# Optimization experiments

Hardware: AMD Instinct MI355X
Metric: run time of the kernel (lower is better)

The kernel has to match this reference:

```python
import jax, jax.numpy as jnp
import numpy as np

N = 131072          # number of feature vectors
F_DIM = 512         # feature_dim
D = 256             # latent_dim
K = 2048            # num_embeddings
BETA = 0.25         # commitment_cost


def _mlp(x, params):
    # params: list of (W, b); ReLU after every layer (matches nn.Sequential)
    for W, b in params:
        x = jax.nn.relu(x @ W + b)
    return x


def setup_inputs() -> dict:
    key = jax.random.key(0)
    ks = jax.random.split(key, 14)

    def lin(k, fan_in, fan_out):
        bound = 1.0 / np.sqrt(fan_in)
        kw, kb = jax.random.split(k)
        W = jax.random.uniform(kw, (fan_in, fan_out), jnp.float32, -bound, bound)
        b = jax.random.uniform(kb, (fan_out,), jnp.float32, -bound, bound)
        return W, b

    enc_w1, enc_b1 = lin(ks[1], F_DIM, 64)
    enc_w2, enc_b2 = lin(ks[2], 64, 128)
    enc_w3, enc_b3 = lin(ks[3], 128, D)
    dec_w1, dec_b1 = lin(ks[4], D, 128)
    dec_w2, dec_b2 = lin(ks[5], 128, 64)
    dec_w3, dec_b3 = lin(ks[6], 64, F_DIM)
    emb = jax.random.uniform(ks[7], (K, D), jnp.float32, -1.0 / K, 1.0 / K)
    x = jax.random.normal(ks[0], (N, F_DIM), jnp.float32)
    return {
        "x": x,
        "enc_w1": enc_w1, "enc_b1": enc_b1,
        "enc_w2": enc_w2, "enc_b2": enc_b2,
        "enc_w3": enc_w3, "enc_b3": enc_b3,
        "dec_w1": dec_w1, "dec_b1": dec_b1,
        "dec_w2": dec_w2, "dec_b2": dec_b2,
        "dec_w3": dec_w3, "dec_b3": dec_b3,
        "emb": emb,
    }


def reference(x, enc_w1, enc_b1, enc_w2, enc_b2, enc_w3, enc_b3,
              dec_w1, dec_b1, dec_w2, dec_b2, dec_w3, dec_b3, emb):
    enc = [(enc_w1, enc_b1), (enc_w2, enc_b2), (enc_w3, enc_b3)]
    dec = [(dec_w1, dec_b1), (dec_w2, dec_b2), (dec_w3, dec_b3)]

    z_e = _mlp(x, enc)  # (N, D)

    # ||z - e||^2 = ||z||^2 - 2 z.e + ||e||^2   (avoids (N,K,D) broadcast)
    z_sq = jnp.sum(z_e * z_e, axis=-1, keepdims=True)      # (N, 1)
    e_sq = jnp.sum(emb * emb, axis=-1)                      # (K,)
    distances = z_sq - 2.0 * (z_e @ emb.T) + e_sq           # (N, K)
    idx = jnp.argmin(distances, axis=1)                     # (N,)
    z_q = emb[idx]                                          # (N, D)

    commitment_loss = BETA * jnp.mean((jax.lax.stop_gradient(z_q) - z_e) ** 2)
    embedding_loss = jnp.mean((z_q - jax.lax.stop_gradient(z_e)) ** 2)
    quantization_loss = embedding_loss + commitment_loss

    # straight-through estimator
    z_q_st = z_e + jax.lax.stop_gradient(z_q - z_e)

    x_recon = _mlp(z_q_st, dec)
    recon_loss = jnp.mean((x_recon - x) ** 2)
    loss = recon_loss + quantization_loss

    z_latent = jax.lax.stop_gradient(z_q_st)
    return (z_latent, loss)
```

## Files before the change

### kernel.cpp

```cpp
#include <hip/hip_runtime.h>

#define NROWS 131072
#define KE 2048
#define CAND_CAP 8192

typedef unsigned long long u64_t;
typedef unsigned int u32;
typedef __attribute__((ext_vector_type(8))) short bf16x8;
typedef __attribute__((ext_vector_type(4))) float f32x4;

__device__ __forceinline__ unsigned f32_key(float f) {
  unsigned u = __float_as_uint(f);
  return (u & 0x80000000u) ? ~u : (u | 0x80000000u);
}

template <int MODE>
__global__ __launch_bounds__(256) void gemm64(
    const float* __restrict__ A, const float* __restrict__ B,
    const float* __restrict__ bias, float* __restrict__ C,
    int M, int N, int K,
    const int* __restrict__ gidx) {
  __shared__ __align__(16) float As[16][68];
  __shared__ __align__(16) float Bs[16][68];

  const int tid = threadIdx.x;
  const int tx = tid & 15;
  const int ty = tid >> 4;
  const int arow = blockIdx.x * 64;
  const int bcol = blockIdx.y * 64;

  const int lr = tid >> 2;
  const int lc = (tid & 3) * 4;
  int ga = arow + lr;
  if (MODE == 1) ga = gidx[ga];
  const float* Ap = A + (size_t)ga * K + lc;

  const int bkr = tid >> 4;
  const int bc4 = (tid & 15) * 4;
  const float* Bp = B + (size_t)bkr * N + bcol + bc4;

  float acc[4][4] = {};

  for (int kt = 0; kt < K; kt += 16) {
    float4 av = *reinterpret_cast<const float4*>(Ap);
    As[lc + 0][lr] = av.x;
    As[lc + 1][lr] = av.y;
    As[lc + 2][lr] = av.z;
    As[lc + 3][lr] = av.w;
    float4 bv = *reinterpret_cast<const float4*>(Bp);
    *reinterpret_cast<float4*>(&Bs[bkr][bc4]) = bv;
    Bp += (size_t)16 * N;
    Ap += 16;
    __syncthreads();
#pragma unroll
    for (int k = 0; k < 16; ++k) {
      float4 a = *reinterpret_cast<const float4*>(&As[k][ty * 4]);
      float4 b = *reinterpret_cast<const float4*>(&Bs[k][tx * 4]);
      acc[0][0] += a.x * b.x; acc[0][1] += a.x * b.y; acc[0][2] += a.x * b.z; acc[0][3] += a.x * b.w;
      acc[1][0] += a.y * b.x; acc[1][1] += a.y * b.y; acc[1][2] += a.y * b.z; acc[1][3] += a.y * b.w;
      acc[2][0] += a.z * b.x; acc[2][1] += a.z * b.y; acc[2][2] += a.z * b.z; acc[2][3] += a.z * b.w;
      acc[3][0] += a.w * b.x; acc[3][1] += a.w * b.y; acc[3][2] += a.w * b.z; acc[3][3] += a.w * b.w;
    }
    __syncthreads();
  }

#pragma unroll
  for (int i = 0; i < 4; ++i) {
    const int row = arow + ty * 4 + i;
    float4 v;
    v.x = fmaxf(acc[i][0] + bias[bcol + tx * 4 + 0], 0.f);
    v.y = fmaxf(acc[i][1] + bias[bcol + tx * 4 + 1], 0.f);
    v.z = fmaxf(acc[i][2] + bias[bcol + tx * 4 + 2], 0.f);
    v.w = fmaxf(acc[i][3] + bias[bcol + tx * 4 + 3], 0.f);
    *reinterpret_cast<float4*>(&C[(size_t)row * N + bcol + tx * 4]) = v;
  }
}

template <int MODE>
__global__ __launch_bounds__(256) void gemm128(
    const float* __restrict__ A, const float* __restrict__ B,
    const float* __restrict__ bias, float* __restrict__ C,
    int N, int K,
    const int* __restrict__ gidx,
    const float* __restrict__ X,
    float* __restrict__ parts) {
  __shared__ __align__(16) char smem[17408];
  float (*As)[132] = (float(*)[132])smem;
  float (*Bs)[132] = (float(*)[132])(smem + 8448);

  const int tid = threadIdx.x;
  const int tx = tid & 15;
  const int ty = tid >> 4;
  const int arow = blockIdx.x * 128;
  const int bcol = blockIdx.y * 128;

  const int r0 = tid >> 2;
  const int r1 = r0 + 64;
  const int lc = (tid & 3) * 4;
  int ga0 = arow + r0, ga1 = arow + r1;
  if (MODE == 1) { ga0 = gidx[ga0]; ga1 = gidx[ga1]; }
  const float* Ap0 = A + (size_t)ga0 * K + lc;
  const float* Ap1 = A + (size_t)ga1 * K + lc;

  const int bk0 = tid >> 5;
  const int bc0 = (tid & 31) * 4;
  const float* Bp0 = B + (size_t)bk0 * N + bcol + bc0;
  const float* Bp1 = B + (size_t)(bk0 + 8) * N + bcol + bc0;

  float acc[8][8] = {};

  for (int kt = 0; kt < K; kt += 16) {
    float4 a0 = *reinterpret_cast<const float4*>(Ap0);
    float4 a1 = *reinterpret_cast<const float4*>(Ap1);
    As[lc + 0][r0] = a0.x; As[lc + 1][r0] = a0.y; As[lc + 2][r0] = a0.z; As[lc + 3][r0] = a0.w;
    As[lc + 0][r1] = a1.x; As[lc + 1][r1] = a1.y; As[lc + 2][r1] = a1.z; As[lc + 3][r1] = a1.w;
    float4 b0 = *reinterpret_cast<const float4*>(Bp0);
    float4 b1 = *reinterpret_cast<const float4*>(Bp1);
    *reinterpret_cast<float4*>(&Bs[bk0][bc0]) = b0;
    *reinterpret_cast<float4*>(&Bs[bk0 + 8][bc0]) = b1;
    Bp0 += (size_t)16 * N; Bp1 += (size_t)16 * N;
    Ap0 += 16; Ap1 += 16;
    __syncthreads();
#pragma unroll
    for (int k = 0; k < 16; ++k) {
      float4 av0 = *reinterpret_cast<const float4*>(&As[k][ty * 4]);
      float4 av1 = *reinterpret_cast<const float4*>(&As[k][64 + ty * 4]);
      float4 bv0 = *reinterpret_cast<const float4*>(&Bs[k][tx * 4]);
      float4 bv1 = *reinterpret_cast<const float4*>(&Bs[k][64 + tx * 4]);
      const float a[8] = {av0.x, av0.y, av0.z, av0.w, av1.x, av1.y, av1.z, av1.w};
      const float b[8] = {bv0.x, bv0.y, bv0.z, bv0.w, bv1.x, bv1.y, bv1.z, bv1.w};
#pragma unroll
      for (int i = 0; i < 8; ++i)
#pragma unroll
        for (int j = 0; j < 8; ++j) acc[i][j] += a[i] * b[j];
    }
    __syncthreads();
  }

  if (MODE == 0 || MODE == 1) {
#pragma unroll
    for (int i = 0; i < 8; ++i) {
      const int row = arow + (i >> 2) * 64 + ty * 4 + (i & 3);
      const int c0 = bcol + tx * 4;
      const int c1 = bcol + 64 + tx * 4;
      float4 v0, v1;
      v0.x = fmaxf(acc[i][0] + bias[c0 + 0], 0.f);
      v0.y = fmaxf(acc[i][1] + bias[c0 + 1], 0.f);
      v0.z = fmaxf(acc[i][2] + bias[c0 + 2], 0.f);
      v0.w = fmaxf(acc[i][3] + bias[c0 + 3], 0.f);
      v1.x = fmaxf(acc[i][4] + bias[c1 + 0], 0.f);
      v1.y = fmaxf(acc[i][5] + bias[c1 + 1], 0.f);
      v1.z = fmaxf(acc[i][6] + bias[c1 + 2], 0.f);
      v1.w = fmaxf(acc[i][7] + bias[c1 + 3], 0.f);
      *reinterpret_cast<float4*>(&C[(size_t)row * N + c0]) = v0;
      *reinterpret_cast<float4*>(&C[(size_t)row * N + c1]) = v1;
    }
  } else if (MODE == 2) {
    float local = 0.f;
#pragma unroll
    for (int i = 0; i < 8; ++i) {
      const int row = arow + (i >> 2) * 64 + ty * 4 + (i & 3);
#pragma unroll
      for (int j = 0; j < 8; ++j) {
        const int col = bcol + (j >> 2) * 64 + tx * 4 + (j & 3);
        float v = fmaxf(acc[i][j] + bias[col], 0.f);
        float d = v - X[(size_t)row * N + col];
        local += d * d;
      }
    }
    float* rbuf = (float*)smem;
    rbuf[tid] = local;
    __syncthreads();
    for (int off = 128; off > 0; off >>= 1) {
      if (tid < off) rbuf[tid] += rbuf[tid + off];
      __syncthreads();
    }
    if (tid == 0) parts[blockIdx.y * gridDim.x + blockIdx.x] = rbuf[0];
  }
}

__device__ __forceinline__ unsigned short bf16_rne(float f) {
  unsigned u = __float_as_uint(f);
  u += 0x7FFFu + ((u >> 16) & 1u);
  return (unsigned short)(u >> 16);
}

__global__ __launch_bounds__(256) void cvt_z16t(const float* __restrict__ z_e,
                                                unsigned short* __restrict__ z16t) {
  const int c = blockIdx.x * 256 + threadIdx.x;
  const int lane = c & 63;
  const int kb = (c >> 6) & 7;
  const int fr = (c >> 9) & 3;
  const int w = (c >> 11) & 3;
  const int rowblk = c >> 13;
  const int row = rowblk * 256 + w * 64 + fr * 16 + (lane & 15);
  const int k0 = kb * 32 + (lane >> 4) * 8;
  const float* p = z_e + (size_t)row * 256 + k0;
  const float4 v0 = *reinterpret_cast<const float4*>(p);
  const float4 v1 = *reinterpret_cast<const float4*>(p + 4);
  const float f[8] = {v0.x, v0.y, v0.z, v0.w, v1.x, v1.y, v1.z, v1.w};
  unsigned short s[8];
#pragma unroll
  for (int j = 0; j < 8; ++j) s[j] = bf16_rne(f[j]);
  uint4 o;
  o.x = (u32)s[0] | ((u32)s[1] << 16);
  o.y = (u32)s[2] | ((u32)s[3] << 16);
  o.z = (u32)s[4] | ((u32)s[5] << 16);
  o.w = (u32)s[6] | ((u32)s[7] << 16);
  *reinterpret_cast<uint4*>(z16t + (size_t)c * 8) = o;
}

__global__ __launch_bounds__(256) void cvt_e16f(const float* __restrict__ emb,
                                                unsigned short* __restrict__ e16f) {
  const int c = blockIdx.x * 256 + threadIdx.x;
  const int l = c & 63;
  const int fc = (c >> 6) & 7;
  const int t = c >> 9;
  const int kb = t & 7;
  const int ct = t >> 3;
  const int col = ct * 128 + fc * 16 + (l & 15);
  const int k0 = kb * 32 + (l >> 4) * 8;
  const float* p = emb + (size_t)col * 256 + k0;
  const float4 v0 = *reinterpret_cast<const float4*>(p);
  const float4 v1 = *reinterpret_cast<const float4*>(p + 4);
  const float f[8] = {v0.x, v0.y, v0.z, v0.w, v1.x, v1.y, v1.z, v1.w};
  unsigned short s8[8];
#pragma unroll
  for (int j = 0; j < 8; ++j) s8[j] = bf16_rne(f[j]);
  uint4 o;
  o.x = (u32)s8[0] | ((u32)s8[1] << 16);
  o.y = (u32)s8[2] | ((u32)s8[3] << 16);
  o.z = (u32)s8[4] | ((u32)s8[5] << 16);
  o.w = (u32)s8[6] | ((u32)s8[7] << 16);
  *reinterpret_cast<uint4*>(e16f + (size_t)c * 8) = o;
}

__global__ __launch_bounds__(256, 1) void dist_g256(
    const unsigned short* __restrict__ z16t, const unsigned short* __restrict__ e16f,
    const float* __restrict__ zf, const float* __restrict__ ef,
    const float* __restrict__ zsq, const float* __restrict__ esq,
    const float* __restrict__ maxesq, u64_t* __restrict__ keys) {
  __shared__ float esq_lds[2048];
  __shared__ float me1_lds[256];
  __shared__ float rowmin_lds[256];
  __shared__ unsigned cand[CAND_CAP];
  __shared__ unsigned cnt;

  const int tid = threadIdx.x;
  const int l = tid & 63;
  const int w = tid >> 6;
  const int l15 = tid & 15;
  const int lk = (tid >> 4) & 3;
  const int arow = blockIdx.x * 256;

  if (tid == 0) cnt = 0;
  {
    for (int i = tid; i < 2048; i += 256) esq_lds[i] = esq[i];
    me1_lds[tid] = 0.009765625f * sqrtf(zsq[arow + tid]);
    rowmin_lds[tid] = 3.402823466e38f;
  }
  const float semax = sqrtf(maxesq[0]);

  bf16x8 a[4][8];
  {
    const char* zb = (const char*)z16t + (size_t)blockIdx.x * 131072 + w * 32768 + l * 16;
#pragma unroll
    for (int fr = 0; fr < 4; ++fr)
#pragma unroll
      for (int kb = 0; kb < 8; ++kb)
        a[fr][kb] = *reinterpret_cast<const bf16x8*>(zb + fr * 8192 + kb * 1024);
  }

  auto rescore = [&](unsigned e) {
    const int row = arow + (int)(e >> 11);
    const int col = (int)(e & 2047u);
    const float* zp = zf + (size_t)row * 256;
    const float* ep = ef + (size_t)col * 256;
    float p = 0.f;
#pragma unroll 8
    for (int k4 = 0; k4 < 256; k4 += 4) {
      const float4 zv = *reinterpret_cast<const float4*>(zp + k4);
      const float4 ev = *reinterpret_cast<const float4*>(ep + k4);
      p = fmaf(zv.x, ev.x, p);
      p = fmaf(zv.y, ev.y, p);
      p = fmaf(zv.z, ev.z, p);
      p = fmaf(zv.w, ev.w, p);
    }
    const float dsc = (zsq[row] - 2.f * p) + esq[col];
    const u64_t kk = ((u64_t)f32_key(dsc) << 32) | (unsigned)col;
    atomicMin(&keys[row], kk);
  };

  __syncthreads();

  const char* eb = (const char*)e16f + (size_t)l * 16;
  const int ct0 = (int)((blockIdx.x * 5u) & 15u);

  f32x4 acc[4][8];
#pragma unroll
  for (int fr = 0; fr < 4; ++fr)
#pragma unroll
    for (int fc = 0; fc < 8; ++fc) acc[fr][fc] = (f32x4){0.f, 0.f, 0.f, 0.f};

  bf16x8 bc[8], bn[8];
#pragma unroll
  for (int fc = 0; fc < 8; ++fc)
    bc[fc] = *reinterpret_cast<const bf16x8*>(eb + (size_t)(ct0 * 8) * 8192 + fc * 1024);

#pragma unroll 1
  for (int ctl = 0; ctl < 16; ++ctl) {
    const int ct = (ct0 + ctl) & 15;
#pragma unroll
    for (int kb = 0; kb < 8; ++kb) {
      const int nctl = (kb == 7) ? ctl + 1 : ctl;
      const int nkb = (kb == 7) ? 0 : kb + 1;
      if (nctl < 16) {
        const int nct = (ct0 + nctl) & 15;
        const char* tb = eb + (size_t)(nct * 8 + nkb) * 8192;
#pragma unroll
        for (int fc = 0; fc < 8; ++fc)
          bn[fc] = *reinterpret_cast<const bf16x8*>(tb + fc * 1024);
      }
#pragma unroll
      for (int fr = 0; fr < 4; ++fr)
#pragma unroll
        for (int fc = 0; fc < 8; ++fc)
          acc[fr][fc] = __builtin_amdgcn_mfma_f32_16x16x32_bf16(a[fr][kb], bc[fc], acc[fr][fc], 0, 0, 0);
#pragma unroll
      for (int fc = 0; fc < 8; ++fc) bc[fc] = bn[fc];
    }
    {
      float esqv[8], se[8];
#pragma unroll
      for (int fc = 0; fc < 8; ++fc) {
        esqv[fc] = esq_lds[ct * 128 + fc * 16 + l15];
        se[fc] = sqrtf(esqv[fc]);
      }
#pragma unroll
      for (int fr = 0; fr < 4; ++fr)
#pragma unroll
        for (int rg = 0; rg < 4; ++rg) {
          float s8[8];
          float lm = 3.402823466e38f;
#pragma unroll
          for (int fc = 0; fc < 8; ++fc) {
            s8[fc] = fmaf(-2.f, acc[fr][fc][rg], esqv[fc]);
            lm = fminf(lm, s8[fc]);
          }
#pragma unroll
          for (int m = 1; m < 16; m <<= 1) lm = fminf(lm, __shfl_xor(lm, m, 64));
          const int row = w * 64 + fr * 16 + lk * 4 + rg;
          const float rm = fminf(rowmin_lds[row], lm);
          if (l15 == 0) rowmin_lds[row] = rm;
          const float me1 = me1_lds[row];
#pragma unroll
          for (int fc = 0; fc < 8; ++fc) {
            const float thr = rm + me1 * (se[fc] + semax) + 1e-7f;
            if (s8[fc] <= thr) {
              const unsigned code =
                  ((unsigned)row << 11) | (unsigned)(ct * 128 + fc * 16 + l15);
              const unsigned idx = atomicAdd(&cnt, 1u);
              if (idx < CAND_CAP) cand[idx] = code;
              else rescore(code);
            }
          }
        }
#pragma unroll
      for (int fr = 0; fr < 4; ++fr)
#pragma unroll
        for (int fc = 0; fc < 8; ++fc) acc[fr][fc] = (f32x4){0.f, 0.f, 0.f, 0.f};
    }
  }

  __syncthreads();
  const unsigned nc = cnt < CAND_CAP ? cnt : CAND_CAP;
  for (unsigned i = tid; i < nc; i += 256) rescore(cand[i]);
}

__global__ __launch_bounds__(256) void max_esq(const float* __restrict__ esq,
                                               float* __restrict__ outv) {
  __shared__ float red[256];
  float m = 0.f;
  for (int i = threadIdx.x; i < KE; i += 256) m = fmaxf(m, esq[i]);
  red[threadIdx.x] = m;
  __syncthreads();
  for (int off = 128; off > 0; off >>= 1) {
    if (threadIdx.x < off) red[threadIdx.x] = fmaxf(red[threadIdx.x], red[threadIdx.x + off]);
    __syncthreads();
  }
  if (threadIdx.x == 0) outv[0] = red[0];
}

__global__ __launch_bounds__(256) void rowsq(const float* __restrict__ src,
                                             float* __restrict__ dst, int rows) {
  const int sub = threadIdx.x >> 6;
  const int lane = threadIdx.x & 63;
  const int r = blockIdx.x * 4 + sub;
  if (r >= rows) return;
  const float* p = src + (size_t)r * 256;
  float s = 0.f;
#pragma unroll
  for (int j = 0; j < 4; ++j) {
    float v = p[lane + 64 * j];
    s += v * v;
  }
#pragma unroll
  for (int off = 32; off > 0; off >>= 1) s += __shfl_down(s, off, 64);
  if (lane == 0) dst[r] = s;
}

__global__ __launch_bounds__(256) void init_keys(u64_t* __restrict__ keys) {
  keys[(size_t)blockIdx.x * 256 + threadIdx.x] = ~0ull;
}

__global__ __launch_bounds__(256) void gather_quant(
    const u64_t* __restrict__ keys, const float* __restrict__ emb,
    const float* __restrict__ z_e, float* __restrict__ zlat,
    int* __restrict__ idx_out, float* __restrict__ qparts) {
  const int sub = threadIdx.x >> 6;
  const int lane = threadIdx.x & 63;
  const int r = blockIdx.x * 4 + sub;
  const int idx = (int)(keys[r] & 0xFFFFFFFFull);
  if (lane == 0) idx_out[r] = idx;
  float s = 0.f;
#pragma unroll
  for (int j = 0; j < 4; ++j) {
    const int d = lane + 64 * j;
    float e = emb[(size_t)idx * 256 + d];
    float z = z_e[(size_t)r * 256 + d];
    float df = e - z;
    s += df * df;
    zlat[(size_t)r * 256 + d] = z + df;
  }
#pragma unroll
  for (int off = 32; off > 0; off >>= 1) s += __shfl_down(s, off, 64);
  __shared__ float red[4];
  if (lane == 0) red[sub] = s;
  __syncthreads();
  if (threadIdx.x == 0) qparts[blockIdx.x] = (red[0] + red[1]) + (red[2] + red[3]);
}

__global__ __launch_bounds__(256) void final_loss(
    const float* __restrict__ qparts, int nq,
    const float* __restrict__ rparts, int nr, float* __restrict__ out) {
  const int tid = threadIdx.x;
  double sq = 0.0, sr = 0.0;
  for (int i = tid; i < nq; i += 256) sq += (double)qparts[i];
  for (int i = tid; i < nr; i += 256) sr += (double)rparts[i];
  __shared__ double bq[256], br[256];
  bq[tid] = sq;
  br[tid] = sr;
  __syncthreads();
  for (int off = 128; off > 0; off >>= 1) {
    if (tid < off) {
      bq[tid] += bq[tid + off];
      br[tid] += br[tid + off];
    }
    __syncthreads();
  }
  if (tid == 0) {
    double qm = bq[0] / ((double)NROWS * 256.0);
    double rm = br[0] / ((double)NROWS * 512.0);
    out[(size_t)NROWS * 256] = (float)(rm + 1.25 * qm);
  }
}

extern "C" void kernel_launch(void* const* d_in, const int* in_sizes, int n_in,
                              void* d_out, int out_size, void* d_ws, size_t ws_size,
                              hipStream_t stream) {
  const float* x   = (const float*)d_in[0];
  const float* ew1 = (const float*)d_in[1];
  const float* eb1 = (const float*)d_in[2];
  const float* ew2 = (const float*)d_in[3];
  const float* eb2 = (const float*)d_in[4];
  const float* ew3 = (const float*)d_in[5];
  const float* eb3 = (const float*)d_in[6];
  const float* dw1 = (const float*)d_in[7];
  const float* db1 = (const float*)d_in[8];
  const float* dw2 = (const float*)d_in[9];
  const float* db2 = (const float*)d_in[10];
  const float* dw3 = (const float*)d_in[11];
  const float* db3 = (const float*)d_in[12];
  const float* emb = (const float*)d_in[13];

  char* ws = (char*)d_ws;
  float* h1            = (float*)(ws);
  unsigned short* e16f = (unsigned short*)(ws);
  float* maxesq        = (float*)(ws + 2097152ull);
  float* h2            = (float*)(ws + 33554432ull);
  unsigned short* z16t = (unsigned short*)(ws + 33554432ull);
  float* z_e    = (float*)(ws + 100663296ull);
  float* zsq    = (float*)(ws + 234881024ull);
  float* esq    = (float*)(ws + 235405312ull);
  u64_t* keys   = (u64_t*)(ws + 235413504ull);
  int* idx      = (int*)(ws + 236462080ull);
  float* qparts = (float*)(ws + 236986368ull);
  float* rparts = (float*)(ws + 237117440ull);

  float* out = (float*)d_out;
  dim3 blk(256);

  gemm64<0><<<dim3(NROWS / 64, 1), blk, 0, stream>>>(x, ew1, eb1, h1, NROWS, 64, 512,
      nullptr);
  gemm128<0><<<dim3(NROWS / 128, 1), blk, 0, stream>>>(h1, ew2, eb2, h2,
      128, 64, nullptr, nullptr, nullptr);
  gemm128<0><<<dim3(NROWS / 128, 2), blk, 0, stream>>>(h2, ew3, eb3, z_e,
      256, 128, nullptr, nullptr, nullptr);

  rowsq<<<dim3(NROWS / 4), blk, 0, stream>>>(z_e, zsq, NROWS);
  rowsq<<<dim3(KE / 4), blk, 0, stream>>>(emb, esq, KE);
  max_esq<<<dim3(1), blk, 0, stream>>>(esq, maxesq);
  init_keys<<<dim3(NROWS / 256), blk, 0, stream>>>(keys);

  cvt_z16t<<<dim3(NROWS * 256 / 8 / 256), blk, 0, stream>>>(z_e, z16t);
  cvt_e16f<<<dim3(KE * 256 / 8 / 256), blk, 0, stream>>>(emb, e16f);

  dist_g256<<<dim3(NROWS / 256), blk, 0, stream>>>(z16t, e16f, z_e, emb, zsq, esq,
      maxesq, keys);

  gather_quant<<<dim3(NROWS / 4), blk, 0, stream>>>(keys, emb, z_e, out, idx, qparts);

  gemm128<1><<<dim3(NROWS / 128, 1), blk, 0, stream>>>(emb, dw1, db1, h2,
      128, 256, idx, nullptr, nullptr);
  gemm64<0><<<dim3(NROWS / 64, 1), blk, 0, stream>>>(h2, dw2, db2, h1, NROWS, 64, 128,
      nullptr);
  gemm128<2><<<dim3(NROWS / 128, 4), blk, 0, stream>>>(h1, dw3, db3, nullptr,
      512, 64, nullptr, x, rparts);

  final_loss<<<dim3(1), blk, 0, stream>>>(qparts, NROWS / 4, rparts, 4096, out);
}
```

Baseline: 1.349 ms.

## Run decoder MLP layers on bf16 MFMA with pre-swizzled weight fragments

Replaces the three fp32 SIMT decoder GEMMs with a templated bf16 MFMA kernel. Weights are pre-converted into per-lane fragment layout and held in registers. The A tile is loaded into XOR-swizzled LDS, with the codebook gather fused in for the first layer. Intermediate activations are stored as bf16, which halves traffic, and the last layer fuses the reconstruction loss. This trades decoder precision (bf16 inputs and intermediates) for fewer FLOP-bound cycles and less memory traffic, so the loss may deviate slightly from the fp32 reference.

```diff
diff --git a/kernel.cpp b/kernel.cpp
--- a/kernel.cpp
+++ b/kernel.cpp
@@ -12,6 +12,12 @@
 __device__ __forceinline__ unsigned f32_key(float f) {
   unsigned u = __float_as_uint(f);
   return (u & 0x80000000u) ? ~u : (u | 0x80000000u);
+}
+
+__device__ __forceinline__ unsigned short bf16_rne(float f) {
+  unsigned u = __float_as_uint(f);
+  u += 0x7FFFu + ((u >> 16) & 1u);
+  return (unsigned short)(u >> 16);
 }
 
 template <int MODE>
@@ -137,52 +143,23 @@
     __syncthreads();
   }
 
-  if (MODE == 0 || MODE == 1) {
-#pragma unroll
-    for (int i = 0; i < 8; ++i) {
-      const int row = arow + (i >> 2) * 64 + ty * 4 + (i & 3);
-      const int c0 = bcol + tx * 4;
-      const int c1 = bcol + 64 + tx * 4;
-      float4 v0, v1;
-      v0.x = fmaxf(acc[i][0] + bias[c0 + 0], 0.f);
-      v0.y = fmaxf(acc[i][1] + bias[c0 + 1], 0.f);
-      v0.z = fmaxf(acc[i][2] + bias[c0 + 2], 0.f);
-      v0.w = fmaxf(acc[i][3] + bias[c0 + 3], 0.f);
-      v1.x = fmaxf(acc[i][4] + bias[c1 + 0], 0.f);
-      v1.y = fmaxf(acc[i][5] + bias[c1 + 1], 0.f);
-      v1.z = fmaxf(acc[i][6] + bias[c1 + 2], 0.f);
-      v1.w = fmaxf(acc[i][7] + bias[c1 + 3], 0.f);
-      *reinterpret_cast<float4*>(&C[(size_t)row * N + c0]) = v0;
-      *reinterpret_cast<float4*>(&C[(size_t)row * N + c1]) = v1;
-    }
-  } else if (MODE == 2) {
-    float local = 0.f;
-#pragma unroll
-    for (int i = 0; i < 8; ++i) {
-      const int row = arow + (i >> 2) * 64 + ty * 4 + (i & 3);
-#pragma unroll
-      for (int j = 0; j < 8; ++j) {
-        const int col = bcol + (j >> 2) * 64 + tx * 4 + (j & 3);
-        float v = fmaxf(acc[i][j] + bias[col], 0.f);
-        float d = v - X[(size_t)row * N + col];
-        local += d * d;
-      }
-    }
-    float* rbuf = (float*)smem;
-    rbuf[tid] = local;
-    __syncthreads();
-    for (int off = 128; off > 0; off >>= 1) {
-      if (tid < off) rbuf[tid] += rbuf[tid + off];
-      __syncthreads();
-    }
-    if (tid == 0) parts[blockIdx.y * gridDim.x + blockIdx.x] = rbuf[0];
-  }
-}
-
-__device__ __forceinline__ unsigned short bf16_rne(float f) {
-  unsigned u = __float_as_uint(f);
-  u += 0x7FFFu + ((u >> 16) & 1u);
-  return (unsigned short)(u >> 16);
+#pragma unroll
+  for (int i = 0; i < 8; ++i) {
+    const int row = arow + (i >> 2) * 64 + ty * 4 + (i & 3);
+    const int c0 = bcol + tx * 4;
+    const int c1 = bcol + 64 + tx * 4;
+    float4 v0, v1;
+    v0.x = fmaxf(acc[i][0] + bias[c0 + 0], 0.f);
+    v0.y = fmaxf(acc[i][1] + bias[c0 + 1], 0.f);
+    v0.z = fmaxf(acc[i][2] + bias[c0 + 2], 0.f);
+    v0.w = fmaxf(acc[i][3] + bias[c0 + 3], 0.f);
+    v1.x = fmaxf(acc[i][4] + bias[c1 + 0], 0.f);
+    v1.y = fmaxf(acc[i][5] + bias[c1 + 1], 0.f);
+    v1.z = fmaxf(acc[i][6] + bias[c1 + 2], 0.f);
+    v1.w = fmaxf(acc[i][7] + bias[c1 + 3], 0.f);
+    *reinterpret_cast<float4*>(&C[(size_t)row * N + c0]) = v0;
+    *reinterpret_cast<float4*>(&C[(size_t)row * N + c1]) = v1;
+  }
 }
 
 __global__ __launch_bounds__(256) void cvt_z16t(const float* __restrict__ z_e,
@@ -235,6 +212,46 @@
   *reinterpret_cast<uint4*>(e16f + (size_t)c * 8) = o;
 }
 
+__global__ __launch_bounds__(256) void cvt_rows16(const float* __restrict__ src,
+                                                  unsigned short* __restrict__ dst) {
+  const int i = blockIdx.x * 256 + threadIdx.x;
+  const float4 v0 = *reinterpret_cast<const float4*>(src + (size_t)i * 8);
+  const float4 v1 = *reinterpret_cast<const float4*>(src + (size_t)i * 8 + 4);
+  const float f[8] = {v0.x, v0.y, v0.z, v0.w, v1.x, v1.y, v1.z, v1.w};
+  unsigned short s[8];
+#pragma unroll
+  for (int j = 0; j < 8; ++j) s[j] = bf16_rne(f[j]);
+  uint4 o;
+  o.x = (u32)s[0] | ((u32)s[1] << 16);
+  o.y = (u32)s[2] | ((u32)s[3] << 16);
+  o.z = (u32)s[4] | ((u32)s[5] << 16);
+  o.w = (u32)s[6] | ((u32)s[7] << 16);
+  *reinterpret_cast<uint4*>(dst + (size_t)i * 8) = o;
+}
+
+__global__ __launch_bounds__(256) void cvt_w16f(const float* __restrict__ W,
+                                                unsigned short* __restrict__ Wf,
+                                                int N, int total) {
+  const int c = blockIdx.x * 256 + threadIdx.x;
+  if (c >= total) return;
+  const int l = c & 63;
+  const int f = c >> 6;
+  const int ng = N >> 4;
+  const int cg = f % ng;
+  const int kb = f / ng;
+  const int col = cg * 16 + (l & 15);
+  const int k0 = kb * 32 + ((l >> 4) & 3) * 8;
+  unsigned short s[8];
+#pragma unroll
+  for (int j = 0; j < 8; ++j) s[j] = bf16_rne(W[(size_t)(k0 + j) * N + col]);
+  uint4 o;
+  o.x = (u32)s[0] | ((u32)s[1] << 16);
+  o.y = (u32)s[2] | ((u32)s[3] << 16);
+  o.z = (u32)s[4] | ((u32)s[5] << 16);
+  o.w = (u32)s[6] | ((u32)s[7] << 16);
+  *reinterpret_cast<uint4*>(Wf + (size_t)c * 8) = o;
+}
+
 __global__ __launch_bounds__(256, 1) void dist_g256(
     const unsigned short* __restrict__ z16t, const unsigned short* __restrict__ e16f,
     const float* __restrict__ zf, const float* __restrict__ ef,
@@ -375,6 +392,112 @@
   __syncthreads();
   const unsigned nc = cnt < CAND_CAP ? cnt : CAND_CAP;
   for (unsigned i = tid; i < nc; i += 256) rescore(cand[i]);
+}
+
+template <int K, int NT, int NTOT, bool GATHER, bool LOSS>
+__global__ __launch_bounds__(256, 1) void dec_mfma(
+    const unsigned short* __restrict__ A16, const unsigned short* __restrict__ Wf,
+    const float* __restrict__ bias, unsigned short* __restrict__ C16,
+    const float* __restrict__ X, float* __restrict__ parts,
+    const int* __restrict__ gidx) {
+  constexpr int CH = K / 8;
+  constexpr int KB = K / 32;
+  constexpr int CG = NT / 16;
+  constexpr int NB = NTOT / NT;
+  __shared__ __align__(16) unsigned short Atile[128 * K];
+  __shared__ int idx_l[128];
+  __shared__ float rbuf[256];
+
+  const int tid = threadIdx.x;
+  const int l = tid & 63;
+  const int w = tid >> 6;
+  const int arow = (int)(blockIdx.x / NB) * 128;
+  const int bcol = (int)(blockIdx.x % NB) * NT;
+
+  if (GATHER) {
+    if (tid < 128) idx_l[tid] = gidx[arow + tid];
+    __syncthreads();
+  }
+  for (int q = tid; q < 128 * CH; q += 256) {
+    const int r = q / CH;
+    const int c = q % CH;
+    const unsigned short* src = GATHER
+        ? A16 + (size_t)idx_l[r] * K + c * 8
+        : A16 + (size_t)(arow + r) * K + c * 8;
+    const uint4 v = *reinterpret_cast<const uint4*>(src);
+    *reinterpret_cast<uint4*>(&Atile[(r * CH + (c ^ (r & 7))) * 8]) = v;
+  }
+
+  bf16x8 wf[KB][CG];
+#pragma unroll
+  for (int kb = 0; kb < KB; ++kb)
+#pragma unroll
+    for (int cg = 0; cg < CG; ++cg)
+      wf[kb][cg] = *reinterpret_cast<const bf16x8*>(
+          Wf + ((size_t)(kb * (NTOT / 16) + bcol / 16 + cg) * 64 + l) * 8);
+
+  __syncthreads();
+
+  f32x4 acc[2][CG];
+#pragma unroll
+  for (int fr = 0; fr < 2; ++fr)
+#pragma unroll
+    for (int cg = 0; cg < CG; ++cg) acc[fr][cg] = (f32x4){0.f, 0.f, 0.f, 0.f};
+
+#pragma unroll
+  for (int kb = 0; kb < KB; ++kb) {
+    bf16x8 af[2];
+#pragma unroll
+    for (int fr = 0; fr < 2; ++fr) {
+      const int r = w * 32 + fr * 16 + (l & 15);
+      const int c = (kb * 4 + ((l >> 4) & 3)) ^ (r & 7);
+      af[fr] = *reinterpret_cast<const bf16x8*>(&Atile[(r * CH + c) * 8]);
+    }
+#pragma unroll
+    for (int fr = 0; fr < 2; ++fr)
+#pragma unroll
+      for (int cg = 0; cg < CG; ++cg)
+        acc[fr][cg] = __builtin_amdgcn_mfma_f32_16x16x32_bf16(af[fr], wf[kb][cg], acc[fr][cg], 0, 0, 0);
+  }
+
+  if (!LOSS) {
+#pragma unroll
+    for (int fr = 0; fr < 2; ++fr)
+#pragma unroll
+      for (int cg = 0; cg < CG; ++cg) {
+        const int col = bcol + cg * 16 + (l & 15);
+        const float bv = bias[col];
+#pragma unroll
+        for (int rg = 0; rg < 4; ++rg) {
+          const int row = arow + w * 32 + fr * 16 + ((l >> 4) & 3) * 4 + rg;
+          const float v = fmaxf(acc[fr][cg][rg] + bv, 0.f);
+          C16[(size_t)row * NTOT + col] = bf16_rne(v);
+        }
+      }
+  } else {
+    float local = 0.f;
+#pragma unroll
+    for (int fr = 0; fr < 2; ++fr)
+#pragma unroll
+      for (int cg = 0; cg < CG; ++cg) {
+        const int col = bcol + cg * 16 + (l & 15);
+        const float bv = bias[col];
+#pragma unroll
+        for (int rg = 0; rg < 4; ++rg) {
+          const int row = arow + w * 32 + fr * 16 + ((l >> 4) & 3) * 4 + rg;
+          const float v = fmaxf(acc[fr][cg][rg] + bv, 0.f);
+          const float d = v - X[(size_t)row * NTOT + col];
+          local = fmaf(d, d, local);
+        }
+      }
+    rbuf[tid] = local;
+    __syncthreads();
+    for (int off = 128; off > 0; off >>= 1) {
+      if (tid < off) rbuf[tid] += rbuf[tid + off];
+      __syncthreads();
+    }
+    if (tid == 0) parts[blockIdx.x] = rbuf[0];
+  }
 }
 
 __global__ __launch_bounds__(256) void max_esq(const float* __restrict__ esq,
@@ -487,8 +610,14 @@
   float* h1            = (float*)(ws);
   unsigned short* e16f = (unsigned short*)(ws);
   float* maxesq        = (float*)(ws + 2097152ull);
+  unsigned short* emb16 = (unsigned short*)(ws + 4194304ull);
+  unsigned short* w1f  = (unsigned short*)(ws + 5242880ull);
+  unsigned short* w2f  = (unsigned short*)(ws + 5308416ull);
+  unsigned short* w3f  = (unsigned short*)(ws + 5324800ull);
   float* h2            = (float*)(ws + 33554432ull);
   unsigned short* z16t = (unsigned short*)(ws + 33554432ull);
+  unsigned short* h2_16 = (unsigned short*)(ws + 33554432ull);
+  unsigned short* h1_16 = (unsigned short*)(ws + 67108864ull);
   float* z_e    = (float*)(ws + 100663296ull);
   float* zsq    = (float*)(ws + 234881024ull);
   float* esq    = (float*)(ws + 235405312ull);
@@ -504,6 +633,10 @@
       nullptr);
   gemm128<0><<<dim3(NROWS / 128, 1), blk, 0, stream>>>(h1, ew2, eb2, h2,
       128, 64, nullptr, nullptr, nullptr);
+  cvt_rows16<<<dim3(KE * 256 / 8 / 256), blk, 0, stream>>>(emb, emb16);
+  cvt_w16f<<<dim3(16), blk, 0, stream>>>(dw1, w1f, 128, 4096);
+  cvt_w16f<<<dim3(4), blk, 0, stream>>>(dw2, w2f, 64, 1024);
+  cvt_w16f<<<dim3(16), blk, 0, stream>>>(dw3, w3f, 512, 4096);
   gemm128<0><<<dim3(NROWS / 128, 2), blk, 0, stream>>>(h2, ew3, eb3, z_e,
       256, 128, nullptr, nullptr, nullptr);
 
@@ -520,12 +653,12 @@
 
   gather_quant<<<dim3(NROWS / 4), blk, 0, stream>>>(keys, emb, z_e, out, idx, qparts);
 
-  gemm128<1><<<dim3(NROWS / 128, 1), blk, 0, stream>>>(emb, dw1, db1, h2,
-      128, 256, idx, nullptr, nullptr);
-  gemm64<0><<<dim3(NROWS / 64, 1), blk, 0, stream>>>(h2, dw2, db2, h1, NROWS, 64, 128,
-      nullptr);
-  gemm128<2><<<dim3(NROWS / 128, 4), blk, 0, stream>>>(h1, dw3, db3, nullptr,
-      512, 64, nullptr, x, rparts);
-
-  final_loss<<<dim3(1), blk, 0, stream>>>(qparts, NROWS / 4, rparts, 4096, out);
-}
+  dec_mfma<256, 128, 128, true, false><<<dim3(NROWS / 128), blk, 0, stream>>>(
+      emb16, w1f, db1, h2_16, nullptr, nullptr, idx);
+  dec_mfma<128, 64, 64, false, false><<<dim3(NROWS / 128), blk, 0, stream>>>(
+      h2_16, w2f, db2, h1_16, nullptr, nullptr, nullptr);
+  dec_mfma<64, 256, 512, false, true><<<dim3((NROWS / 128) * 2), blk, 0, stream>>>(
+      h1_16, w3f, db3, nullptr, x, rparts, nullptr);
+
+  final_loss<<<dim3(1), blk, 0, stream>>>(qparts, NROWS / 4, rparts, 2048, out);
+}
```

Measured after the change: 1.193 ms, median of 2. 1.13x faster.
